# Kernel tuning notes

Measured on AMD Instinct MI355X. Metric: run time of the kernel, lower is better.

## Reference

```python
import jax, jax.numpy as jnp
import numpy as np

B, T, D, H = 8, 4096, 256, 256

def setup_inputs() -> dict:
    key = jax.random.key(0)
    ks = jax.random.split(key, 6)
    scale = 1.0 / np.sqrt(D)
    return {
        "x": jax.random.normal(ks[0], (B, T, D), dtype=jnp.float32),
        "h0": jax.random.normal(ks[1], (B, H), dtype=jnp.float32),
        "Wz": jax.random.normal(ks[2], (H, D), dtype=jnp.float32) * scale,
        "bz": jax.random.normal(ks[3], (H,), dtype=jnp.float32) * scale,
        "Wh": jax.random.normal(ks[4], (H, D), dtype=jnp.float32) * scale,
        "bh": jax.random.normal(ks[5], (H,), dtype=jnp.float32) * scale,
    }

def reference(x, h0, Wz, bz, Wh, bh):
    # gate and update depend only on the input (minGRU): compute in one shot
    gate = jax.nn.sigmoid(jnp.einsum("btd,hd->bth", x, Wz) + bz)   # [B,T,H]
    update = jnp.einsum("btd,hd->bth", x, Wh) + bh                  # [B,T,H]

    def step(h, gu):
        g, u = gu
        h_new = (1.0 - g) * h + g * u
        return h_new, h_new

    # scan over time; xs laid out [T,B,H]
    _, hs = jax.lax.scan(step, h0, (jnp.swapaxes(gate, 0, 1), jnp.swapaxes(update, 0, 1)))
    return jnp.swapaxes(hs, 0, 1)  # [B,T,H]
```

## Files before the change

### kernel.cpp

```cpp
#include <hip/hip_runtime.h>
#include <hip/hip_fp16.h>


namespace {
constexpr int kB  = 8;
constexpr int kT  = 4096;
constexpr int kD  = 256;
constexpr int kH  = 256;
constexpr int kBT = kB * kT;

constexpr int TM  = 128;
constexpr int TH  = 64;
constexpr int BK  = 64;
constexpr int kNT = kT / TM;
constexpr int kNChain = kB * (kH / TH);
constexpr int EPS = 66;
}

typedef short s16x8 __attribute__((ext_vector_type(8)));
typedef short s16x4 __attribute__((ext_vector_type(4)));
typedef float f32x4 __attribute__((ext_vector_type(4)));

__device__ __forceinline__ short f2bf(float f) {
    union { float f; unsigned int u; } v; v.f = f;
    unsigned int r = v.u + 0x7fffu + ((v.u >> 16) & 1u);
    return (short)(r >> 16);
}

__device__ __forceinline__ void load_lds16(const void* g, void* l) {
    __builtin_amdgcn_global_load_lds(
        (const __attribute__((address_space(1))) void*)g,
        (__attribute__((address_space(3))) void*)l, 16, 0, 0);
}

__global__ __launch_bounds__(256)
void prologue(const float* __restrict__ x,
              const float* __restrict__ Wz,
              const float* __restrict__ Wh,
              unsigned short* __restrict__ xb,
              unsigned short* __restrict__ wzb,
              unsigned short* __restrict__ whb,
              float4* __restrict__ aggz)
{
    constexpr int X4 = kBT * kD / 4;
    constexpr int W4 = kH  * kD / 4;
    constexpr int Z4 = kNChain * kNT * TH * 8 / 16;
    const int i = blockIdx.x * 256 + threadIdx.x;

    if (i >= X4 + 2 * W4) {
        float4 z; z.x = 0.f; z.y = 0.f; z.z = 0.f; z.w = 0.f;
        aggz[i - (X4 + 2 * W4)] = z;
        return;
    }
    const float* src; unsigned short* dst; int j;
    if (i < X4)           { src = x;  dst = xb;  j = i; }
    else if (i < X4 + W4) { src = Wz; dst = wzb; j = i - X4; }
    else                  { src = Wh; dst = whb; j = i - X4 - W4; }
    const float4 v = ((const float4*)src)[j];
    s16x4 p;
    p[0] = f2bf(v.x); p[1] = f2bf(v.y); p[2] = f2bf(v.z); p[3] = f2bf(v.w);
    ((s16x4*)dst)[j] = p;
}

__global__ __launch_bounds__(256, 4)
void gemm_scan_fused(const unsigned short* __restrict__ xb,
                     const unsigned short* __restrict__ wzb,
                     const unsigned short* __restrict__ whb,
                     const float* __restrict__ bz,
                     const float* __restrict__ bh,
                     const float* __restrict__ h0,
                     unsigned long long* __restrict__ agg,
                     float* __restrict__ out)
{
    __shared__ __align__(16) unsigned char smem[36096];
    unsigned short* Xs  = (unsigned short*)smem;
    unsigned short* Wzs = Xs  + 128 * 64;
    unsigned short* Whs = Wzs + 64 * 64;
    __half* a_lds   = (__half*)smem;
    __half* b_lds   = a_lds + 128 * EPS;
    float2* sub_lds = (float2*)(smem + 33792);
    float*  hs_lds  = (float*)(smem + 35840);

    const int tid  = threadIdx.x;
    const int lane = tid & 63;
    const int wv   = tid >> 6;
    const int ln15 = lane & 15;
    const int quad = lane >> 4;
    const int wr0  = (wv & 1) * 64;
    const int wc0  = (wv >> 1) * 32;

    const int chain = blockIdx.x;
    const int t     = blockIdx.y;
    const int b     = chain >> 2;
    const int col0  = (chain & 3) * TH;
    const int row0  = b * kT + t * TM;

    const int srow = lane >> 3;
    const int sk   = (lane & 7) * 8;

    f32x4 accZ[4][2] = {};
    f32x4 accU[4][2] = {};

    for (int k0 = 0; k0 < kD; k0 += BK) {
        #pragma unroll
        for (int s = 0; s < 4; ++s) {
            const int seg = wv * 4 + s;
            const int m = seg * 8 + srow;
            load_lds16(xb + (size_t)(row0 + m) * kD + k0 + sk, Xs + seg * 512);
        }
        #pragma unroll
        for (int s = 0; s < 2; ++s) {
            const int seg = wv * 2 + s;
            const int m = seg * 8 + srow;
            load_lds16(wzb + (size_t)(col0 + m) * kD + k0 + sk, Wzs + seg * 512);
            load_lds16(whb + (size_t)(col0 + m) * kD + k0 + sk, Whs + seg * 512);
        }
        __syncthreads();

        #pragma unroll
        for (int kk = 0; kk < BK; kk += 32) {
            s16x8 af[4], bzf[2], buf[2];
            #pragma unroll
            for (int mt = 0; mt < 4; ++mt)
                af[mt] = *(const s16x8*)&Xs[(wr0 + mt * 16 + ln15) * 64 + kk + quad * 8];
            #pragma unroll
            for (int nt = 0; nt < 2; ++nt) {
                bzf[nt] = *(const s16x8*)&Wzs[(wc0 + nt * 16 + ln15) * 64 + kk + quad * 8];
                buf[nt] = *(const s16x8*)&Whs[(wc0 + nt * 16 + ln15) * 64 + kk + quad * 8];
            }
            #pragma unroll
            for (int mt = 0; mt < 4; ++mt) {
                #pragma unroll
                for (int nt = 0; nt < 2; ++nt) {
                    accZ[mt][nt] = __builtin_amdgcn_mfma_f32_16x16x32_bf16(
                        af[mt], bzf[nt], accZ[mt][nt], 0, 0, 0);
                    accU[mt][nt] = __builtin_amdgcn_mfma_f32_16x16x32_bf16(
                        af[mt], buf[nt], accU[mt][nt], 0, 0, 0);
                }
            }
        }
        __syncthreads();
    }

    #pragma unroll
    for (int nt = 0; nt < 2; ++nt) {
        const int col = col0 + wc0 + nt * 16 + ln15;
        const int lc  = wc0 + nt * 16 + ln15;
        const float bzv = bz[col];
        const float bhv = bh[col];
        #pragma unroll
        for (int mt = 0; mt < 4; ++mt) {
            const int rb = wr0 + mt * 16 + quad * 4;
            #pragma unroll
            for (int r = 0; r < 4; ++r) {
                const float z = accZ[mt][nt][r] + bzv;
                const float g = 1.0f / (1.0f + __expf(-z));
                const float u = accU[mt][nt][r] + bhv;
                a_lds[(rb + r) * EPS + lc] = __float2half_rn(1.0f - g);
                b_lds[(rb + r) * EPS + lc] = __float2half_rn(g * u);
            }
        }
    }
    __syncthreads();

    const int s = tid >> 6;
    const int h = tid & 63;
    {
        float A = 1.0f, Bv = 0.0f;
        #pragma unroll 8
        for (int r = s * 32; r < s * 32 + 32; ++r) {
            const float a  = __half2float(a_lds[r * EPS + h]);
            const float bb = __half2float(b_lds[r * EPS + h]);
            Bv = fmaf(a, Bv, bb);
            A *= a;
        }
        float2 o; o.x = A; o.y = Bv;
        sub_lds[s * 64 + h] = o;
    }
    __syncthreads();

    if (tid < 64) {
        float A = 1.0f, Bv = 0.0f;
        #pragma unroll
        for (int s2 = 0; s2 < 4; ++s2) {
            const float2 g = sub_lds[s2 * 64 + tid];
            Bv = fmaf(g.x, Bv, g.y);
            A *= g.x;
        }
        union { float2 f; unsigned long long u; } pk;
        pk.f.x = A; pk.f.y = Bv;
        pk.u |= 1ull;
        __hip_atomic_store(&agg[(size_t)(chain * kNT + t) * 64 + tid], pk.u,
                           __ATOMIC_RELAXED, __HIP_MEMORY_SCOPE_AGENT);

        float hs = h0[(size_t)b * kH + col0 + tid];
        for (int j = 0; j < t; ++j) {
            unsigned long long u;
            do {
                u = __hip_atomic_load(&agg[(size_t)(chain * kNT + j) * 64 + tid],
                                      __ATOMIC_RELAXED, __HIP_MEMORY_SCOPE_AGENT);
            } while (u == 0ull);
            union { unsigned long long u; float2 f; } qk; qk.u = u;
            hs = fmaf(qk.f.x, hs, qk.f.y);
        }
        hs_lds[tid] = hs;
    }
    __syncthreads();

    {
        float hv = hs_lds[h];
        #pragma unroll
        for (int s2 = 0; s2 < s; ++s2) {
            const float2 g = sub_lds[s2 * 64 + h];
            hv = fmaf(g.x, hv, g.y);
        }
        #pragma unroll 8
        for (int r = 0; r < 32; ++r) {
            const int lr = s * 32 + r;
            const float a  = __half2float(a_lds[lr * EPS + h]);
            const float bb = __half2float(b_lds[lr * EPS + h]);
            hv = fmaf(a, hv, bb);
            out[(size_t)(row0 + lr) * kH + col0 + h] = hv;
        }
    }
}

extern "C" void kernel_launch(void* const* d_in, const int* in_sizes, int n_in,
                              void* d_out, int out_size, void* d_ws, size_t ws_size,
                              hipStream_t stream)
{
    const float* x  = (const float*)d_in[0];
    const float* h0 = (const float*)d_in[1];
    const float* Wz = (const float*)d_in[2];
    const float* bz = (const float*)d_in[3];
    const float* Wh = (const float*)d_in[4];
    const float* bh = (const float*)d_in[5];
    float* out = (float*)d_out;

    unsigned char* ws = (unsigned char*)d_ws;
    unsigned short* xb  = (unsigned short*)ws;   ws += (size_t)kBT * kD * 2;
    unsigned short* wzb = (unsigned short*)ws;   ws += (size_t)kH * kD * 2;
    unsigned short* whb = (unsigned short*)ws;   ws += (size_t)kH * kD * 2;
    unsigned long long* agg = (unsigned long long*)ws;

    constexpr int PRO_ITEMS = kBT * kD / 4 + 2 * (kH * kD / 4)
                            + kNChain * kNT * TH * 8 / 16;
    prologue<<<PRO_ITEMS / 256, 256, 0, stream>>>(
        x, Wz, Wh, xb, wzb, whb, (float4*)agg);
    gemm_scan_fused<<<dim3(kNChain, kNT), 256, 0, stream>>>(
        xb, wzb, whb, bz, bh, h0, agg, out);
}
```

Measured before the change: 118.1 us.

## Swizzle X tile in LDS, read weights from global, batch lookback loads

The GEMM K-tile grows to 128. Only X is staged in LDS, using an XOR-swizzled layout to avoid bank conflicts, and the Wz/Wh fragments are loaded directly from global memory and cache instead of through LDS. The decoupled-lookback loop now issues up to 8 aggregate loads at once before spinning on each, which cuts serialized latency. Output stores become nontemporal. Direct global weight loads may add latency or redundant traffic across blocks, and the larger X tile must still fit within the existing shared buffer.

```diff
diff --git a/kernel.cpp b/kernel.cpp
--- a/kernel.cpp
+++ b/kernel.cpp
@@ -11,7 +11,7 @@
 
 constexpr int TM  = 128;
 constexpr int TH  = 64;
-constexpr int BK  = 64;
+constexpr int BK  = 128;
 constexpr int kNT = kT / TM;
 constexpr int kNChain = kB * (kH / TH);
 constexpr int EPS = 66;
@@ -44,7 +44,6 @@
 {
     constexpr int X4 = kBT * kD / 4;
     constexpr int W4 = kH  * kD / 4;
-    constexpr int Z4 = kNChain * kNT * TH * 8 / 16;
     const int i = blockIdx.x * 256 + threadIdx.x;
 
     if (i >= X4 + 2 * W4) {
@@ -73,9 +72,7 @@
                      float* __restrict__ out)
 {
     __shared__ __align__(16) unsigned char smem[36096];
-    unsigned short* Xs  = (unsigned short*)smem;
-    unsigned short* Wzs = Xs  + 128 * 64;
-    unsigned short* Whs = Wzs + 64 * 64;
+    unsigned short* Xs = (unsigned short*)smem;
     __half* a_lds   = (__half*)smem;
     __half* b_lds   = a_lds + 128 * EPS;
     float2* sub_lds = (float2*)(smem + 33792);
@@ -95,38 +92,39 @@
     const int col0  = (chain & 3) * TH;
     const int row0  = b * kT + t * TM;
 
-    const int srow = lane >> 3;
-    const int sk   = (lane & 7) * 8;
+    const int srow4 = lane >> 4;
+    const int slot  = lane & 15;
 
     f32x4 accZ[4][2] = {};
     f32x4 accU[4][2] = {};
 
     for (int k0 = 0; k0 < kD; k0 += BK) {
         #pragma unroll
-        for (int s = 0; s < 4; ++s) {
-            const int seg = wv * 4 + s;
-            const int m = seg * 8 + srow;
-            load_lds16(xb + (size_t)(row0 + m) * kD + k0 + sk, Xs + seg * 512);
-        }
-        #pragma unroll
-        for (int s = 0; s < 2; ++s) {
-            const int seg = wv * 2 + s;
-            const int m = seg * 8 + srow;
-            load_lds16(wzb + (size_t)(col0 + m) * kD + k0 + sk, Wzs + seg * 512);
-            load_lds16(whb + (size_t)(col0 + m) * kD + k0 + sk, Whs + seg * 512);
+        for (int s = 0; s < 8; ++s) {
+            const int seg = wv * 8 + s;
+            const int m   = seg * 4 + srow4;
+            const int c   = slot ^ (m & 15);
+            load_lds16(xb + (size_t)(row0 + m) * kD + k0 + c * 8,
+                       Xs + seg * 512);
         }
         __syncthreads();
 
         #pragma unroll
         for (int kk = 0; kk < BK; kk += 32) {
-            s16x8 af[4], bzf[2], buf[2];
-            #pragma unroll
-            for (int mt = 0; mt < 4; ++mt)
-                af[mt] = *(const s16x8*)&Xs[(wr0 + mt * 16 + ln15) * 64 + kk + quad * 8];
+            const int cbase = kk >> 3;
+            s16x8 af[4];
+            #pragma unroll
+            for (int mt = 0; mt < 4; ++mt) {
+                const int r = wr0 + mt * 16 + ln15;
+                af[mt] = *(const s16x8*)&Xs[r * 128 + (((cbase + quad) ^ ln15) << 3)];
+            }
+            s16x8 bzf[2], buf[2];
             #pragma unroll
             for (int nt = 0; nt < 2; ++nt) {
-                bzf[nt] = *(const s16x8*)&Wzs[(wc0 + nt * 16 + ln15) * 64 + kk + quad * 8];
-                buf[nt] = *(const s16x8*)&Whs[(wc0 + nt * 16 + ln15) * 64 + kk + quad * 8];
+                const size_t wrow = (size_t)(col0 + wc0 + nt * 16 + ln15) * kD
+                                  + k0 + kk + quad * 8;
+                bzf[nt] = *(const s16x8*)(wzb + wrow);
+                buf[nt] = *(const s16x8*)(whb + wrow);
             }
             #pragma unroll
             for (int mt = 0; mt < 4; ++mt) {
@@ -194,14 +192,26 @@
                            __ATOMIC_RELAXED, __HIP_MEMORY_SCOPE_AGENT);
 
         float hs = h0[(size_t)b * kH + col0 + tid];
-        for (int j = 0; j < t; ++j) {
-            unsigned long long u;
-            do {
-                u = __hip_atomic_load(&agg[(size_t)(chain * kNT + j) * 64 + tid],
-                                      __ATOMIC_RELAXED, __HIP_MEMORY_SCOPE_AGENT);
-            } while (u == 0ull);
-            union { unsigned long long u; float2 f; } qk; qk.u = u;
-            hs = fmaf(qk.f.x, hs, qk.f.y);
+        for (int j0 = 0; j0 < t; j0 += 8) {
+            const int nb = (t - j0 < 8) ? (t - j0) : 8;
+            unsigned long long u[8];
+            #pragma unroll
+            for (int q = 0; q < 8; ++q)
+                if (q < nb)
+                    u[q] = __hip_atomic_load(
+                        &agg[(size_t)(chain * kNT + j0 + q) * 64 + tid],
+                        __ATOMIC_RELAXED, __HIP_MEMORY_SCOPE_AGENT);
+            #pragma unroll
+            for (int q = 0; q < 8; ++q) {
+                if (q < nb) {
+                    while (u[q] == 0ull)
+                        u[q] = __hip_atomic_load(
+                            &agg[(size_t)(chain * kNT + j0 + q) * 64 + tid],
+                            __ATOMIC_RELAXED, __HIP_MEMORY_SCOPE_AGENT);
+                    union { unsigned long long u; float2 f; } qk; qk.u = u[q];
+                    hs = fmaf(qk.f.x, hs, qk.f.y);
+                }
+            }
         }
         hs_lds[tid] = hs;
     }
@@ -220,7 +230,7 @@
             const float a  = __half2float(a_lds[lr * EPS + h]);
             const float bb = __half2float(b_lds[lr * EPS + h]);
             hv = fmaf(a, hv, bb);
-            out[(size_t)(row0 + lr) * kH + col0 + h] = hv;
+            __builtin_nontemporal_store(hv, &out[(size_t)(row0 + lr) * kH + col0 + h]);
         }
     }
 }
```

After: 128.3 us. 8.7% more time.
